# Kernel tuning notes

Measured on AMD Instinct MI355X. Metric: run time of the kernel, lower is better.

## Reference

```python
import jax, jax.numpy as jnp
import numpy as np

# --- constants hardcoded in the torch Model ---
VIEWS = [45.0, 90.0, 135.0, 225.0, 270.0, 315.0]
DIST, ELEV = 1.5, 15.0          # look_at_view_transform(1.5, 15, views)
S = 128                          # image_size
K = 5                            # points_per_pixel
RADIUS = 0.01                    # NDC radius
R2 = RADIUS * RADIUS
ZNEAR, ZFAR = 0.01, 100.0        # FoVOrthographicCameras defaults
BIG = 1e9                        # depth sentinel for non-covering points


def look_at_RT():
    """PyTorch3D look_at_view_transform: world->view is X @ R + T."""
    azim = jnp.deg2rad(jnp.asarray(VIEWS, jnp.float32))
    elev = jnp.deg2rad(jnp.float32(ELEV))
    # camera centers [V,3]
    C = DIST * jnp.stack([jnp.cos(elev) * jnp.sin(azim),
                          jnp.sin(elev) * jnp.ones_like(azim),
                          jnp.cos(elev) * jnp.cos(azim)], axis=-1)
    up = jnp.broadcast_to(jnp.asarray([0.0, 1.0, 0.0], jnp.float32), C.shape)
    z = -C / jnp.linalg.norm(C, axis=-1, keepdims=True)          # at(=0) - eye
    x = jnp.cross(up, z)
    x = x / jnp.linalg.norm(x, axis=-1, keepdims=True)
    y = jnp.cross(z, x)
    y = y / jnp.linalg.norm(y, axis=-1, keepdims=True)
    R = jnp.stack([x, y, z], axis=-1)                            # [V,3,3] cols = axes
    T = -jnp.einsum('vj,vji->vi', C, R)                          # camera -> origin
    return R, T


def render_view(R, T, pts, feats):
    """PointsRasterizer + AlphaCompositor for one FoVOrthographic camera.
    pts [N,3] world, feats [N,3]. Returns image [S,S,3]."""
    pv = pts @ R + T                                             # [N,3] view space
    px, py, pz = pv[:, 0], pv[:, 1], pv[:, 2]
    # orthographic NDC with max_x=max_y=1, min=-1, scale=1 -> ndc_xy == view_xy
    valid = (pz > ZNEAR) & (pz < ZFAR)
    # PyTorch3D pixel centers: PixToNdc(i,S)=(2i+1-S)/S, with x and y flipped
    pix = (2.0 * jnp.arange(S, dtype=pts.dtype) + 1.0 - S) / S
    xf = pix[::-1]                                               # +X is left
    yf = pix[::-1]                                               # +Y is up (row 0 = top)
    dx = xf[None, :, None] - px[None, None, :]                   # [1,S,N]
    dy = yf[:, None, None] - py[None, None, :]                   # [S,1,N]
    d2 = dx * dx + dy * dy                                       # [S,S,N]
    hit = (d2 < R2) & valid[None, None, :]
    score = jnp.where(hit, pz[None, None, :], BIG)               # sort hits by depth
    neg_z, idx = jax.lax.top_k(-score, K)                        # K nearest, [S,S,K]
    ok = (-neg_z) < 0.5 * BIG
    d2k = jnp.take_along_axis(d2, idx, axis=-1)                  # [S,S,K]
    w = jnp.where(ok, 1.0 - d2k / R2, 0.0)                       # alphas in (0,1]
    fk = feats[idx]                                              # [S,S,K,3]
    # front-to-back alpha compositing: sum_k w_k * prod_{j<k}(1-w_j) * f_k
    trans = jnp.cumprod(1.0 - w, axis=-1)
    prefix = jnp.concatenate([jnp.ones_like(w[..., :1]), trans[..., :-1]], axis=-1)
    img = jnp.einsum('hwk,hwkc->hwc', w * prefix, fk)            # background = 0
    return img


def setup_inputs() -> dict:
    key = jax.random.key(0)
    k1, k2 = jax.random.split(key)
    pcd = 0.3 * jax.random.normal(k1, (4096, 3), dtype=jnp.float32)  # inside NDC window
    init_colors = jnp.zeros((4096,), dtype=jnp.float32)
    displace = jax.random.normal(k2, (4096,), dtype=jnp.float32)
    return {"pcd": pcd, "init_colors": init_colors, "displace": displace}


def reference(pcd, init_colors, displace):
    colors_ = jax.nn.sigmoid(init_colors + displace)             # [N]
    feats = jnp.broadcast_to(colors_[:, None], (colors_.shape[0], 3))  # repeat to 3 ch
    R, T = look_at_RT()
    images = jax.lax.map(lambda rt: render_view(rt[0], rt[1], pcd, feats), (R, T))
    return images, colors_                                       # [6,128,128,3], [4096]
```

## Files before the change

### kernel.cpp

```cpp
#include <hip/hip_runtime.h>
#include <hip/hip_bf16.h>
#include <math.h>

#define NPTS 4096
#define SDIM 128
#define NV 6
#define KTOP 5
#define IMG_ELEMS (NV * SDIM * SDIM * 3)

#define R2F 1e-4f
#define RMARG 0.0102f

#define RB 16
#define NBLK (NV * 64)
#define NCELL 16
#define CAPS 256

struct CamParams { float R[NV][9]; float T[NV][3]; };

__device__ __forceinline__ void process_cand(
    float4 P, float xf, float yf,
    float zk[KTOP], float wk[KTOP], float ck[KTOP]) {
  float dx = xf - P.x;
  float dy = yf - P.y;
  float d2 = dx * dx + dy * dy;
  if (d2 < R2F) {
    float wgt = 1.0f - d2 / R2F;
    float z = P.z;
    if (z < zk[KTOP - 1]) {
      zk[KTOP - 1] = z; wk[KTOP - 1] = wgt; ck[KTOP - 1] = P.w;
#pragma unroll
      for (int k = KTOP - 1; k > 0; k--) {
        if (zk[k] < zk[k - 1]) {
          float tz = zk[k]; zk[k] = zk[k - 1]; zk[k - 1] = tz;
          float tw = wk[k]; wk[k] = wk[k - 1]; wk[k - 1] = tw;
          float tc = ck[k]; ck[k] = ck[k - 1]; ck[k - 1] = tc;
        }
      }
    }
  }
}

__global__ __launch_bounds__(256) void fused_render_kernel(
    const float4* __restrict__ pcd4,
    const float4* __restrict__ add0_4,
    const float4* __restrict__ add1_4,
    float* __restrict__ out,
    float4* __restrict__ out_colors4,
    CamParams cams) {
  int b = blockIdx.x;
  int v = b >> 6;
  int t = b & 63;
  int ty = t >> 3, tx = t & 7;
  int tid = threadIdx.x;
  int w0 = tx * RB, h0 = ty * RB;
  int h = h0 + (tid >> 4);
  int w = w0 + (tid & 15);
  float xf = (float)(127 - 2 * w) * (1.0f / 128.0f);
  float yf = (float)(127 - 2 * h) * (1.0f / 128.0f);

  float xhi = (float)(127 - 2 * w0) * (1.0f / 128.0f) + RMARG;
  float xlo = (float)(127 - 2 * (w0 + RB - 1)) * (1.0f / 128.0f) - RMARG;
  float yhi = (float)(127 - 2 * h0) * (1.0f / 128.0f) + RMARG;
  float ylo = (float)(127 - 2 * (h0 + RB - 1)) * (1.0f / 128.0f) - RMARG;

  __shared__ float4 cand[NCELL][CAPS + 1];
  __shared__ int cnts[NCELL];
  if (tid < NCELL) cnts[tid] = 0;
  __syncthreads();

  const float* Rp = cams.R[v];
  const float* Tp = cams.T[v];
  float R0 = Rp[0], R1 = Rp[1], R2 = Rp[2];
  float R3 = Rp[3], R4 = Rp[4], R5 = Rp[5];
  float R6 = Rp[6], R7 = Rp[7], R8 = Rp[8];
  float T0 = Tp[0], T1 = Tp[1], T2 = Tp[2];

  float4 A[4][3], C0[4], C1[4];
#pragma unroll
  for (int k = 0; k < 4; k++) {
    int g = k * 256 + tid;
    A[k][0] = pcd4[3 * g + 0];
    A[k][1] = pcd4[3 * g + 1];
    A[k][2] = pcd4[3 * g + 2];
    C0[k] = add0_4[g];
    C1[k] = add1_4[g];
  }

#pragma unroll
  for (int k = 0; k < 4; k++) {
    float f[12] = {A[k][0].x, A[k][0].y, A[k][0].z, A[k][0].w,
                   A[k][1].x, A[k][1].y, A[k][1].z, A[k][1].w,
                   A[k][2].x, A[k][2].y, A[k][2].z, A[k][2].w};
    float4 s;
    s.x = 1.0f / (1.0f + expf(-(C0[k].x + C1[k].x)));
    s.y = 1.0f / (1.0f + expf(-(C0[k].y + C1[k].y)));
    s.z = 1.0f / (1.0f + expf(-(C0[k].z + C1[k].z)));
    s.w = 1.0f / (1.0f + expf(-(C0[k].w + C1[k].w)));
    if (b == k) out_colors4[k * 256 + tid] = s;
    float sc[4] = {s.x, s.y, s.z, s.w};
#pragma unroll
    for (int j = 0; j < 4; j++) {
      float p0 = f[3 * j + 0], p1 = f[3 * j + 1], p2 = f[3 * j + 2];
      float px = p0 * R0 + p1 * R3 + p2 * R6 + T0;
      float py = p0 * R1 + p1 * R4 + p2 * R7 + T1;
      float pz = p0 * R2 + p1 * R5 + p2 * R8 + T2;
      if (pz > 0.01f && pz < 100.0f &&
          px > xlo && px < xhi && py > ylo && py < yhi) {
        float lwlo = (127.0f - 128.0f * (px + RMARG)) * 0.5f - (float)w0;
        float lwhi = (127.0f - 128.0f * (px - RMARG)) * 0.5f - (float)w0;
        float lhlo = (127.0f - 128.0f * (py + RMARG)) * 0.5f - (float)h0;
        float lhhi = (127.0f - 128.0f * (py - RMARG)) * 0.5f - (float)h0;
        int cxlo = (int)fmaxf(0.0f, floorf(lwlo * 0.25f));
        int cxhi = (int)fminf(3.0f, floorf(lwhi * 0.25f));
        int cylo = (int)fmaxf(0.0f, floorf(lhlo * 0.25f));
        int cyhi = (int)fminf(3.0f, floorf(lhhi * 0.25f));
        float4 payload = make_float4(px, py, pz, sc[j]);
        for (int cy = cylo; cy <= cyhi; cy++)
          for (int cx = cxlo; cx <= cxhi; cx++) {
            int li = cy * 4 + cx;
            int idx = atomicAdd(&cnts[li], 1);
            if (idx < CAPS) cand[li][idx] = payload;
          }
      }
    }
  }
  __syncthreads();

  int li = (tid >> 6) * 4 + ((tid >> 2) & 3);
  int n = cnts[li];
  if (n > CAPS) n = CAPS;
  const float4* list = cand[li];

  float zk[KTOP], wk[KTOP], ck[KTOP];
#pragma unroll
  for (int k = 0; k < KTOP; k++) { zk[k] = 1e30f; wk[k] = 0.0f; ck[k] = 0.0f; }

  int j = 0;
  for (; j + 4 <= n; j += 4) {
    float4 P0 = list[j + 0];
    float4 P1 = list[j + 1];
    float4 P2 = list[j + 2];
    float4 P3 = list[j + 3];
    process_cand(P0, xf, yf, zk, wk, ck);
    process_cand(P1, xf, yf, zk, wk, ck);
    process_cand(P2, xf, yf, zk, wk, ck);
    process_cand(P3, xf, yf, zk, wk, ck);
  }
  for (; j < n; j++) {
    float4 P = list[j];
    process_cand(P, xf, yf, zk, wk, ck);
  }

  float acc = 0.0f, pre = 1.0f;
#pragma unroll
  for (int k = 0; k < KTOP; k++) {
    acc += wk[k] * pre * ck[k];
    pre *= (1.0f - wk[k]);
  }

  int base = v * (SDIM * SDIM * 3) + (h * SDIM + w) * 3;
  out[base + 0] = acc;
  out[base + 1] = acc;
  out[base + 2] = acc;
}

static void compute_cams(CamParams* cp) {
  const double views[NV] = {45.0, 90.0, 135.0, 225.0, 270.0, 315.0};
  const double deg = M_PI / 180.0;
  const double elev = 15.0 * deg;
  const double dist = 1.5;
  for (int v = 0; v < NV; v++) {
    double az = views[v] * deg;
    double C[3] = {dist * cos(elev) * sin(az), dist * sin(elev),
                   dist * cos(elev) * cos(az)};
    double n = sqrt(C[0] * C[0] + C[1] * C[1] + C[2] * C[2]);
    double z[3] = {-C[0] / n, -C[1] / n, -C[2] / n};
    double up[3] = {0.0, 1.0, 0.0};
    double x[3] = {up[1] * z[2] - up[2] * z[1],
                   up[2] * z[0] - up[0] * z[2],
                   up[0] * z[1] - up[1] * z[0]};
    double nx = sqrt(x[0] * x[0] + x[1] * x[1] + x[2] * x[2]);
    x[0] /= nx; x[1] /= nx; x[2] /= nx;
    double y[3] = {z[1] * x[2] - z[2] * x[1],
                   z[2] * x[0] - z[0] * x[2],
                   z[0] * x[1] - z[1] * x[0]};
    double ny = sqrt(y[0] * y[0] + y[1] * y[1] + y[2] * y[2]);
    y[0] /= ny; y[1] /= ny; y[2] /= ny;
    double Rm[3][3];
    for (int j = 0; j < 3; j++) { Rm[j][0] = x[j]; Rm[j][1] = y[j]; Rm[j][2] = z[j]; }
    for (int j = 0; j < 3; j++)
      for (int i = 0; i < 3; i++)
        cp->R[v][j * 3 + i] = (float)Rm[j][i];
    for (int i = 0; i < 3; i++)
      cp->T[v][i] = (float)(-(C[0] * Rm[0][i] + C[1] * Rm[1][i] + C[2] * Rm[2][i]));
  }
}

extern "C" void kernel_launch(void* const* d_in, const int* in_sizes, int n_in,
                              void* d_out, int out_size, void* d_ws, size_t ws_size,
                              hipStream_t stream) {
  CamParams cp;
  compute_cams(&cp);

  const float* pcd = nullptr;
  const float* adds[2] = {nullptr, nullptr};
  int na = 0;
  for (int i = 0; i < n_in; i++) {
    if (in_sizes[i] == 3 * NPTS) pcd = (const float*)d_in[i];
    else if (na < 2) adds[na++] = (const float*)d_in[i];
  }
  if (!pcd || na < 2) { pcd = (const float*)d_in[0];
                        adds[0] = (const float*)d_in[1];
                        adds[1] = (const float*)d_in[2]; }

  float* out = (float*)d_out;
  float4* out_colors4 = (float4*)(out + IMG_ELEMS);

  fused_render_kernel<<<NBLK, 256, 0, stream>>>(
      (const float4*)pcd, (const float4*)adds[0], (const float4*)adds[1],
      out, out_colors4, cp);
}
```

Before: 80.08 us.

## Use 32x16 pixel tiles with 512-thread blocks and fast sigmoid

Result: faster. 75.21 us (median of 2 runs) (-6.1%).

```diff
diff --git a/kernel.cpp b/kernel.cpp
--- a/kernel.cpp
+++ b/kernel.cpp
@@ -11,12 +11,19 @@
 #define R2F 1e-4f
 #define RMARG 0.0102f
 
-#define RB 16
-#define NBLK (NV * 64)
-#define NCELL 16
-#define CAPS 256
+#define RBW 32
+#define RBH 16
+#define NBLK (NV * 32)
+#define NCX 8
+#define NCY 4
+#define NCELL 32
+#define CAPS 128
 
 struct CamParams { float R[NV][9]; float T[NV][3]; };
+
+__device__ __forceinline__ float sigmoidf_fast(float x) {
+  return __fdividef(1.0f, 1.0f + __expf(-x));
+}
 
 __device__ __forceinline__ void process_cand(
     float4 P, float xf, float yf,
@@ -41,7 +48,7 @@
   }
 }
 
-__global__ __launch_bounds__(256) void fused_render_kernel(
+__global__ __launch_bounds__(512) void fused_render_kernel(
     const float4* __restrict__ pcd4,
     const float4* __restrict__ add0_4,
     const float4* __restrict__ add1_4,
@@ -49,20 +56,21 @@
     float4* __restrict__ out_colors4,
     CamParams cams) {
   int b = blockIdx.x;
-  int v = b >> 6;
-  int t = b & 63;
-  int ty = t >> 3, tx = t & 7;
+  int v = b >> 5;
+  int t = b & 31;
+  int ty = t >> 2, tx = t & 3;
   int tid = threadIdx.x;
-  int w0 = tx * RB, h0 = ty * RB;
-  int h = h0 + (tid >> 4);
-  int w = w0 + (tid & 15);
+  int w0 = tx * RBW, h0 = ty * RBH;
+  int row = tid >> 5, col = tid & 31;
+  int h = h0 + row;
+  int w = w0 + col;
   float xf = (float)(127 - 2 * w) * (1.0f / 128.0f);
   float yf = (float)(127 - 2 * h) * (1.0f / 128.0f);
 
   float xhi = (float)(127 - 2 * w0) * (1.0f / 128.0f) + RMARG;
-  float xlo = (float)(127 - 2 * (w0 + RB - 1)) * (1.0f / 128.0f) - RMARG;
+  float xlo = (float)(127 - 2 * (w0 + RBW - 1)) * (1.0f / 128.0f) - RMARG;
   float yhi = (float)(127 - 2 * h0) * (1.0f / 128.0f) + RMARG;
-  float ylo = (float)(127 - 2 * (h0 + RB - 1)) * (1.0f / 128.0f) - RMARG;
+  float ylo = (float)(127 - 2 * (h0 + RBH - 1)) * (1.0f / 128.0f) - RMARG;
 
   __shared__ float4 cand[NCELL][CAPS + 1];
   __shared__ int cnts[NCELL];
@@ -76,10 +84,10 @@
   float R6 = Rp[6], R7 = Rp[7], R8 = Rp[8];
   float T0 = Tp[0], T1 = Tp[1], T2 = Tp[2];
 
-  float4 A[4][3], C0[4], C1[4];
-#pragma unroll
-  for (int k = 0; k < 4; k++) {
-    int g = k * 256 + tid;
+  float4 A[2][3], C0[2], C1[2];
+#pragma unroll
+  for (int k = 0; k < 2; k++) {
+    int g = k * 512 + tid;
     A[k][0] = pcd4[3 * g + 0];
     A[k][1] = pcd4[3 * g + 1];
     A[k][2] = pcd4[3 * g + 2];
@@ -87,18 +95,25 @@
     C1[k] = add1_4[g];
   }
 
-#pragma unroll
-  for (int k = 0; k < 4; k++) {
+  if (b < 2) {
+    int g = b * 512 + tid;
+    float4 s;
+    s.x = sigmoidf_fast(C0[b].x + C1[b].x);
+    s.y = sigmoidf_fast(C0[b].y + C1[b].y);
+    s.z = sigmoidf_fast(C0[b].z + C1[b].z);
+    s.w = sigmoidf_fast(C0[b].w + C1[b].w);
+    out_colors4[g] = s;
+  }
+
+#pragma unroll
+  for (int k = 0; k < 2; k++) {
     float f[12] = {A[k][0].x, A[k][0].y, A[k][0].z, A[k][0].w,
                    A[k][1].x, A[k][1].y, A[k][1].z, A[k][1].w,
                    A[k][2].x, A[k][2].y, A[k][2].z, A[k][2].w};
-    float4 s;
-    s.x = 1.0f / (1.0f + expf(-(C0[k].x + C1[k].x)));
-    s.y = 1.0f / (1.0f + expf(-(C0[k].y + C1[k].y)));
-    s.z = 1.0f / (1.0f + expf(-(C0[k].z + C1[k].z)));
-    s.w = 1.0f / (1.0f + expf(-(C0[k].w + C1[k].w)));
-    if (b == k) out_colors4[k * 256 + tid] = s;
-    float sc[4] = {s.x, s.y, s.z, s.w};
+    float sc[4] = {sigmoidf_fast(C0[k].x + C1[k].x),
+                   sigmoidf_fast(C0[k].y + C1[k].y),
+                   sigmoidf_fast(C0[k].z + C1[k].z),
+                   sigmoidf_fast(C0[k].w + C1[k].w)};
 #pragma unroll
     for (int j = 0; j < 4; j++) {
       float p0 = f[3 * j + 0], p1 = f[3 * j + 1], p2 = f[3 * j + 2];
@@ -112,13 +127,13 @@
         float lhlo = (127.0f - 128.0f * (py + RMARG)) * 0.5f - (float)h0;
         float lhhi = (127.0f - 128.0f * (py - RMARG)) * 0.5f - (float)h0;
         int cxlo = (int)fmaxf(0.0f, floorf(lwlo * 0.25f));
-        int cxhi = (int)fminf(3.0f, floorf(lwhi * 0.25f));
+        int cxhi = (int)fminf((float)(NCX - 1), floorf(lwhi * 0.25f));
         int cylo = (int)fmaxf(0.0f, floorf(lhlo * 0.25f));
-        int cyhi = (int)fminf(3.0f, floorf(lhhi * 0.25f));
+        int cyhi = (int)fminf((float)(NCY - 1), floorf(lhhi * 0.25f));
         float4 payload = make_float4(px, py, pz, sc[j]);
         for (int cy = cylo; cy <= cyhi; cy++)
           for (int cx = cxlo; cx <= cxhi; cx++) {
-            int li = cy * 4 + cx;
+            int li = cy * NCX + cx;
             int idx = atomicAdd(&cnts[li], 1);
             if (idx < CAPS) cand[li][idx] = payload;
           }
@@ -127,7 +142,7 @@
   }
   __syncthreads();
 
-  int li = (tid >> 6) * 4 + ((tid >> 2) & 3);
+  int li = (row >> 2) * NCX + (col >> 2);
   int n = cnts[li];
   if (n > CAPS) n = CAPS;
   const float4* list = cand[li];
@@ -137,15 +152,17 @@
   for (int k = 0; k < KTOP; k++) { zk[k] = 1e30f; wk[k] = 0.0f; ck[k] = 0.0f; }
 
   int j = 0;
-  for (; j + 4 <= n; j += 4) {
-    float4 P0 = list[j + 0];
-    float4 P1 = list[j + 1];
-    float4 P2 = list[j + 2];
-    float4 P3 = list[j + 3];
+  for (; j + 8 <= n; j += 8) {
+    float4 P0 = list[j + 0], P1 = list[j + 1], P2 = list[j + 2], P3 = list[j + 3];
+    float4 P4 = list[j + 4], P5 = list[j + 5], P6 = list[j + 6], P7 = list[j + 7];
     process_cand(P0, xf, yf, zk, wk, ck);
     process_cand(P1, xf, yf, zk, wk, ck);
     process_cand(P2, xf, yf, zk, wk, ck);
     process_cand(P3, xf, yf, zk, wk, ck);
+    process_cand(P4, xf, yf, zk, wk, ck);
+    process_cand(P5, xf, yf, zk, wk, ck);
+    process_cand(P6, xf, yf, zk, wk, ck);
+    process_cand(P7, xf, yf, zk, wk, ck);
   }
   for (; j < n; j++) {
     float4 P = list[j];
@@ -217,7 +234,7 @@
   float* out = (float*)d_out;
   float4* out_colors4 = (float4*)(out + IMG_ELEMS);
 
-  fused_render_kernel<<<NBLK, 256, 0, stream>>>(
+  fused_render_kernel<<<NBLK, 512, 0, stream>>>(
       (const float4*)pcd, (const float4*)adds[0], (const float4*)adds[1],
       out, out_colors4, cp);
 }
```

## Use 32x32 pixel tiles with 1024-thread blocks and 32 binning cells

Applied to the files above, without the earlier changes.

Result: no change. 79.55 us (-0.7%).

```diff
diff --git a/kernel.cpp b/kernel.cpp
--- a/kernel.cpp
+++ b/kernel.cpp
@@ -11,12 +11,18 @@
 #define R2F 1e-4f
 #define RMARG 0.0102f
 
-#define RB 16
-#define NBLK (NV * 64)
-#define NCELL 16
-#define CAPS 256
+#define RB 32
+#define NBLK (NV * 16)
+#define NCX 4
+#define NCY 8
+#define NCELL 32
+#define CAPS 126
 
 struct CamParams { float R[NV][9]; float T[NV][3]; };
+
+__device__ __forceinline__ float sigmoidf_fast(float x) {
+  return __fdividef(1.0f, 1.0f + __expf(-x));
+}
 
 __device__ __forceinline__ void process_cand(
     float4 P, float xf, float yf,
@@ -41,7 +47,7 @@
   }
 }
 
-__global__ __launch_bounds__(256) void fused_render_kernel(
+__global__ __launch_bounds__(1024) void fused_render_kernel(
     const float4* __restrict__ pcd4,
     const float4* __restrict__ add0_4,
     const float4* __restrict__ add1_4,
@@ -49,13 +55,14 @@
     float4* __restrict__ out_colors4,
     CamParams cams) {
   int b = blockIdx.x;
-  int v = b >> 6;
-  int t = b & 63;
-  int ty = t >> 3, tx = t & 7;
+  int v = b >> 4;
+  int t = b & 15;
+  int ty = t >> 2, tx = t & 3;
   int tid = threadIdx.x;
+  int row = tid >> 5, col = tid & 31;
   int w0 = tx * RB, h0 = ty * RB;
-  int h = h0 + (tid >> 4);
-  int w = w0 + (tid & 15);
+  int h = h0 + row;
+  int w = w0 + col;
   float xf = (float)(127 - 2 * w) * (1.0f / 128.0f);
   float yf = (float)(127 - 2 * h) * (1.0f / 128.0f);
 
@@ -76,58 +83,51 @@
   float R6 = Rp[6], R7 = Rp[7], R8 = Rp[8];
   float T0 = Tp[0], T1 = Tp[1], T2 = Tp[2];
 
-  float4 A[4][3], C0[4], C1[4];
-#pragma unroll
-  for (int k = 0; k < 4; k++) {
-    int g = k * 256 + tid;
-    A[k][0] = pcd4[3 * g + 0];
-    A[k][1] = pcd4[3 * g + 1];
-    A[k][2] = pcd4[3 * g + 2];
-    C0[k] = add0_4[g];
-    C1[k] = add1_4[g];
-  }
-
-#pragma unroll
-  for (int k = 0; k < 4; k++) {
-    float f[12] = {A[k][0].x, A[k][0].y, A[k][0].z, A[k][0].w,
-                   A[k][1].x, A[k][1].y, A[k][1].z, A[k][1].w,
-                   A[k][2].x, A[k][2].y, A[k][2].z, A[k][2].w};
-    float4 s;
-    s.x = 1.0f / (1.0f + expf(-(C0[k].x + C1[k].x)));
-    s.y = 1.0f / (1.0f + expf(-(C0[k].y + C1[k].y)));
-    s.z = 1.0f / (1.0f + expf(-(C0[k].z + C1[k].z)));
-    s.w = 1.0f / (1.0f + expf(-(C0[k].w + C1[k].w)));
-    if (b == k) out_colors4[k * 256 + tid] = s;
-    float sc[4] = {s.x, s.y, s.z, s.w};
-#pragma unroll
-    for (int j = 0; j < 4; j++) {
-      float p0 = f[3 * j + 0], p1 = f[3 * j + 1], p2 = f[3 * j + 2];
-      float px = p0 * R0 + p1 * R3 + p2 * R6 + T0;
-      float py = p0 * R1 + p1 * R4 + p2 * R7 + T1;
-      float pz = p0 * R2 + p1 * R5 + p2 * R8 + T2;
-      if (pz > 0.01f && pz < 100.0f &&
-          px > xlo && px < xhi && py > ylo && py < yhi) {
-        float lwlo = (127.0f - 128.0f * (px + RMARG)) * 0.5f - (float)w0;
-        float lwhi = (127.0f - 128.0f * (px - RMARG)) * 0.5f - (float)w0;
-        float lhlo = (127.0f - 128.0f * (py + RMARG)) * 0.5f - (float)h0;
-        float lhhi = (127.0f - 128.0f * (py - RMARG)) * 0.5f - (float)h0;
-        int cxlo = (int)fmaxf(0.0f, floorf(lwlo * 0.25f));
-        int cxhi = (int)fminf(3.0f, floorf(lwhi * 0.25f));
-        int cylo = (int)fmaxf(0.0f, floorf(lhlo * 0.25f));
-        int cyhi = (int)fminf(3.0f, floorf(lhhi * 0.25f));
-        float4 payload = make_float4(px, py, pz, sc[j]);
-        for (int cy = cylo; cy <= cyhi; cy++)
-          for (int cx = cxlo; cx <= cxhi; cx++) {
-            int li = cy * 4 + cx;
-            int idx = atomicAdd(&cnts[li], 1);
-            if (idx < CAPS) cand[li][idx] = payload;
-          }
-      }
+  int g = tid;
+  float4 a0 = pcd4[3 * g + 0];
+  float4 a1 = pcd4[3 * g + 1];
+  float4 a2 = pcd4[3 * g + 2];
+  float4 c0 = add0_4[g];
+  float4 c1 = add1_4[g];
+
+  float f[12] = {a0.x, a0.y, a0.z, a0.w,
+                 a1.x, a1.y, a1.z, a1.w,
+                 a2.x, a2.y, a2.z, a2.w};
+  float sc[4] = {sigmoidf_fast(c0.x + c1.x),
+                 sigmoidf_fast(c0.y + c1.y),
+                 sigmoidf_fast(c0.z + c1.z),
+                 sigmoidf_fast(c0.w + c1.w)};
+
+  if (b == 0) out_colors4[g] = make_float4(sc[0], sc[1], sc[2], sc[3]);
+
+#pragma unroll
+  for (int j = 0; j < 4; j++) {
+    float p0 = f[3 * j + 0], p1 = f[3 * j + 1], p2 = f[3 * j + 2];
+    float px = p0 * R0 + p1 * R3 + p2 * R6 + T0;
+    float py = p0 * R1 + p1 * R4 + p2 * R7 + T1;
+    float pz = p0 * R2 + p1 * R5 + p2 * R8 + T2;
+    if (pz > 0.01f && pz < 100.0f &&
+        px > xlo && px < xhi && py > ylo && py < yhi) {
+      float lwlo = (127.0f - 128.0f * (px + RMARG)) * 0.5f - (float)w0;
+      float lwhi = (127.0f - 128.0f * (px - RMARG)) * 0.5f - (float)w0;
+      float lhlo = (127.0f - 128.0f * (py + RMARG)) * 0.5f - (float)h0;
+      float lhhi = (127.0f - 128.0f * (py - RMARG)) * 0.5f - (float)h0;
+      int cxlo = (int)fmaxf(0.0f, floorf(lwlo * 0.125f));
+      int cxhi = (int)fminf((float)(NCX - 1), floorf(lwhi * 0.125f));
+      int cylo = (int)fmaxf(0.0f, floorf(lhlo * 0.25f));
+      int cyhi = (int)fminf((float)(NCY - 1), floorf(lhhi * 0.25f));
+      float4 payload = make_float4(px, py, pz, sc[j]);
+      for (int cy = cylo; cy <= cyhi; cy++)
+        for (int cx = cxlo; cx <= cxhi; cx++) {
+          int li = cy * NCX + cx;
+          int idx = atomicAdd(&cnts[li], 1);
+          if (idx < CAPS) cand[li][idx] = payload;
+        }
     }
   }
   __syncthreads();
 
-  int li = (tid >> 6) * 4 + ((tid >> 2) & 3);
+  int li = (row >> 2) * NCX + (col >> 3);
   int n = cnts[li];
   if (n > CAPS) n = CAPS;
   const float4* list = cand[li];
@@ -138,10 +138,8 @@
 
   int j = 0;
   for (; j + 4 <= n; j += 4) {
-    float4 P0 = list[j + 0];
-    float4 P1 = list[j + 1];
-    float4 P2 = list[j + 2];
-    float4 P3 = list[j + 3];
+    float4 P0 = list[j + 0], P1 = list[j + 1];
+    float4 P2 = list[j + 2], P3 = list[j + 3];
     process_cand(P0, xf, yf, zk, wk, ck);
     process_cand(P1, xf, yf, zk, wk, ck);
     process_cand(P2, xf, yf, zk, wk, ck);
@@ -217,7 +215,7 @@
   float* out = (float*)d_out;
   float4* out_colors4 = (float4*)(out + IMG_ELEMS);
 
-  fused_render_kernel<<<NBLK, 256, 0, stream>>>(
+  fused_render_kernel<<<NBLK, 1024, 0, stream>>>(
       (const float4*)pcd, (const float4*)adds[0], (const float4*)adds[1],
       out, out_colors4, cp);
 }
```
